# Kernel optimization log

Hardware: AMD Instinct MI355X
Metric: run time of the kernel (lower is better)

Reference implementation:

```python
import jax, jax.numpy as jnp
import numpy as np

B, N, M, D = 64, 512, 1024, 128

def setup_inputs() -> dict:
    key = jax.random.key(0)
    ks = jax.random.split(key, 7)
    s = 1.0 / np.sqrt(D)
    return {
        "h_c": jax.random.normal(ks[0], (B, N, D), dtype=jnp.float32),
        "h_p": jax.random.normal(ks[1], (B, M, D), dtype=jnp.float32),
        "U_w": jax.random.normal(ks[2], (D, D), dtype=jnp.float32) * s,
        "U_b": jax.random.normal(ks[3], (D,), dtype=jnp.float32) * s,
        "V_w": jax.random.normal(ks[4], (D, D), dtype=jnp.float32) * s,
        "V_b": jax.random.normal(ks[5], (D,), dtype=jnp.float32) * s,
        "q": jax.random.normal(ks[6], (D,), dtype=jnp.float32),
    }

def reference(h_c, h_p, U_w, U_b, V_w, V_b, q):
    # ReLU-activated linear projections (torch Linear: x @ W.T + b)
    Uc = jax.nn.relu(jnp.einsum('bnd,ed->bne', h_c, U_w) + U_b)  # (B,N,D)
    Vp = jax.nn.relu(jnp.einsum('bmd,ed->bme', h_p, V_w) + V_b)  # (B,M,D)
    # bilinear attention scores and softmax over protein axis
    attn = jnp.einsum('bnd,bmd->bnm', Uc, Vp)                    # (B,N,M)
    weights = jax.nn.softmax(attn, axis=-1)
    context = jnp.einsum('bnm,bmd->bnd', weights, Vp)            # (B,N,D)
    joint = (Uc + context) * q                                   # (B,N,D)
    return joint.mean(axis=1)                                    # (B,D)
```

## Files before the change

kernel.cpp:

```cpp
#include <hip/hip_runtime.h>
#include <hip/hip_bf16.h>
#include <cstdint>

#define BB 64
#define NN 512
#define MM 1024
#define DD 128

typedef __bf16 bf16x8 __attribute__((ext_vector_type(8)));
typedef float f32x4 __attribute__((ext_vector_type(4)));
typedef short s16x4 __attribute__((ext_vector_type(4)));

static __device__ __forceinline__ unsigned short f2bf(float f) {
    union { float f; unsigned int i; } v; v.f = f;
    unsigned int x = v.i;
    x += 0x7FFFu + ((x >> 16) & 1u);
    return (unsigned short)(x >> 16);
}
static __device__ __forceinline__ unsigned int f2bf2(float a, float b) {
    union { __hip_bfloat162 h; unsigned int u; } c;
    c.h = __float22bfloat162_rn(make_float2(a, b));
    return c.u;
}
static __device__ __forceinline__ void async16(const void* g, void* l) {
    __builtin_amdgcn_global_load_lds(
        (const __attribute__((address_space(1))) void*)g,
        (__attribute__((address_space(3))) void*)l, 16, 0, 0);
}

__global__ __launch_bounds__(256, 4) void proj_kernel(
    const float* __restrict__ hp,
    const float* __restrict__ hc,
    const float* __restrict__ Wu,
    const float* __restrict__ Wv,
    const float* __restrict__ Ub,
    const float* __restrict__ Vb,
    unsigned short* __restrict__ Y,
    unsigned short* __restrict__ YT,
    unsigned short* __restrict__ Ucg,
    float* __restrict__ colsum)
{
    __shared__ __align__(16) unsigned short Ws[128 * 136];
    unsigned short* Ys = Ws;
    unsigned short* Ts = Ws + 8192;
    const int t = threadIdx.x;
    const int lane = t & 63;
    const int wave = t >> 6;
    const int n16 = lane & 15, q = lane >> 4;
    const bool isC = blockIdx.x >= (BB * MM / 64);
    const float ws = isC ? 1.44269504088896f : 1.0f;

    const long row0 = isC ? (long)(blockIdx.x - BB * MM / 64) * 64
                          : (long)blockIdx.x * 64;
    const float* X = isC ? hc : hp;
    const float* Wf = isC ? Wu : Wv;
    const float* bias = isC ? Ub : Vb;

    float4 xv[8];
    {
        const float* xrow = X + (row0 + wave * 16 + n16) * DD + q * 8;
        #pragma unroll
        for (int kk = 0; kk < 4; ++kk) {
            xv[2 * kk]     = *(const float4*)(xrow + kk * 32);
            xv[2 * kk + 1] = *(const float4*)(xrow + kk * 32 + 4);
        }
    }
    {
        const float4* Wg = (const float4*)Wf;
        #pragma unroll
        for (int i = 0; i < 16; ++i) {
            int idx = i * 256 + t;
            float4 v = Wg[idx];
            int off = idx * 4;
            uint2 u = { f2bf2(v.x * ws, v.y * ws), f2bf2(v.z * ws, v.w * ws) };
            *(uint2*)&Ws[(off >> 7) * 136 + (off & 127)] = u;
        }
    }
    __syncthreads();

    f32x4 acc[8];
    #pragma unroll
    for (int j = 0; j < 8; ++j) acc[j] = {0.f, 0.f, 0.f, 0.f};

    #pragma unroll
    for (int kk = 0; kk < 4; ++kk) {
        float4 x0 = xv[2 * kk], x1 = xv[2 * kk + 1];
        union { bf16x8 v; unsigned int u[4]; } a;
        a.u[0] = f2bf2(x0.x, x0.y); a.u[1] = f2bf2(x0.z, x0.w);
        a.u[2] = f2bf2(x1.x, x1.y); a.u[3] = f2bf2(x1.z, x1.w);
        #pragma unroll
        for (int j = 0; j < 8; ++j) {
            bf16x8 b = *(const bf16x8*)&Ws[(j * 16 + n16) * 136 + q * 8 + kk * 32];
            acc[j] = __builtin_amdgcn_mfma_f32_16x16x32_bf16(a.v, b, acc[j], 0, 0, 0);
        }
    }

    unsigned short yb[8][4];
    float colp[8];
    #pragma unroll
    for (int j = 0; j < 8; ++j) {
        const float bv = bias[j * 16 + n16] * ws;
        float y[4], s = 0.f;
        #pragma unroll
        for (int r = 0; r < 4; ++r) {
            float v = acc[j][r] + bv;
            v = v > 0.f ? v : 0.f;
            y[r] = v;
            s += v;
        }
        colp[j] = s;
        uint2 u = { f2bf2(y[0], y[1]), f2bf2(y[2], y[3]) };
        *(uint2*)&yb[j][0] = u;
    }
    __syncthreads();

    if (!isC) {
        #pragma unroll
        for (int j = 0; j < 8; ++j) {
            const int e = j * 16 + n16;
            const int ehi = e >> 3, elo = e & 7;
            #pragma unroll
            for (int r = 0; r < 4; ++r) {
                int row = wave * 16 + q * 4 + r;
                Ys[row * 128 + ((ehi ^ (row & 7)) << 3) + elo] = yb[j][r];
            }
            *(uint2*)&Ts[e * 72 + wave * 16 + q * 4] = *(uint2*)&yb[j][0];
        }
        __syncthreads();
        uint4* dstY = (uint4*)(Y + row0 * DD);
        const long b = row0 >> 10;
        const long mt = (row0 & 1023) >> 6;
        uint4* dstT = (uint4*)(YT + ((b * 16 + mt) * 128) * 64);
        #pragma unroll
        for (int i = 0; i < 4; ++i) {
            int idx = i * 256 + t;
            dstY[idx] = ((const uint4*)Ys)[idx];
            int e = idx >> 3, m = (idx & 7) * 8;
            dstT[idx] = *(const uint4*)&Ts[e * 72 + m];
        }
    } else {
        #pragma unroll
        for (int j = 0; j < 8; ++j) {
            colp[j] += __shfl_xor(colp[j], 16);
            colp[j] += __shfl_xor(colp[j], 32);
        }
        float* cs = (float*)Ts;
        if (q == 0) {
            #pragma unroll
            for (int j = 0; j < 8; ++j)
                cs[wave * 128 + j * 16 + n16] = colp[j];
        }
        #pragma unroll
        for (int j = 0; j < 8; ++j) {
            const int e = j * 16 + n16;
            #pragma unroll
            for (int r = 0; r < 4; ++r)
                Ys[(wave * 16 + q * 4 + r) * 128 + e] = yb[j][r];
        }
        __syncthreads();
        const int c = (int)(row0 >> 6);
        uint4* dstU = (uint4*)(Ucg + row0 * DD);
        #pragma unroll
        for (int i = 0; i < 4; ++i) {
            int idx = i * 256 + t;
            dstU[idx] = ((const uint4*)Ys)[idx];
        }
        if (t < 128)
            colsum[(long)c * DD + t] = cs[t] + cs[128 + t] + cs[256 + t] + cs[384 + t];
    }
}

__global__ __launch_bounds__(256, 2) void attn_kernel(
    const unsigned short* __restrict__ Ucg,
    const unsigned short* __restrict__ Vp,
    const unsigned short* __restrict__ VpT,
    float* __restrict__ part)
{
    __shared__ __align__(16) unsigned short smem[32768];

    const int t = threadIdx.x;
    const int lane = t & 63;
    const int wave = t >> 6;
    const int n16 = lane & 15, q = lane >> 4;

    const int id = blockIdx.x;
    const int xcd = id & 7;
    const int slot = id >> 3;
    const int b = xcd * 8 + (slot >> 3);
    const int nt = slot & 7;

    const unsigned short* vpb = Vp + (long)b * MM * DD;
    const unsigned short* vtb = VpT + (long)b * MM * DD;
    const unsigned short* ucb = Ucg + ((long)b * NN + nt * 64) * DD;

    bf16x8 Bn[4];
    #pragma unroll
    for (int kk = 0; kk < 4; ++kk)
        Bn[kk] = *(const bf16x8*)&ucb[(wave * 16 + n16) * 128 + kk * 32 + q * 8];

    {
        #pragma unroll
        for (int i = 0; i < 4; ++i) {
            int L = wave * 256 + i * 64 + lane;
            async16(vpb + L * 8, smem + wave * 2048 + i * 512);
        }
        #pragma unroll
        for (int i = 0; i < 4; ++i) {
            int L = wave * 256 + i * 64 + lane;
            int r = L >> 3, sc = L & 7, c = sc ^ (r & 7);
            async16(vtb + r * 64 + c * 8, smem + 16384 + wave * 2048 + i * 512);
        }
    }
    asm volatile("s_waitcnt vmcnt(0) lgkmcnt(0)" ::: "memory");
    __builtin_amdgcn_s_barrier();
    __builtin_amdgcn_sched_barrier(0);

    f32x4 O[8];
    #pragma unroll
    for (int j = 0; j < 8; ++j) O[j] = {0.f, 0.f, 0.f, 0.f};
    float lsum = 0.f;

    #pragma unroll 1
    for (int mt = 0; mt < 16; ++mt) {
        const unsigned short* V  = (mt & 1) ? smem + 8192  : smem;
        const unsigned short* VT = (mt & 1) ? smem + 24576 : smem + 16384;
        if (mt < 15) {
            const unsigned short* sv = vpb + (mt + 1) * 8192;
            const unsigned short* st = vtb + (mt + 1) * 8192;
            unsigned short* dv = ((mt & 1) ? smem : smem + 8192) + wave * 2048;
            unsigned short* dt = ((mt & 1) ? smem + 16384 : smem + 24576) + wave * 2048;
            #pragma unroll
            for (int i = 0; i < 4; ++i) {
                int L = wave * 256 + i * 64 + lane;
                async16(sv + L * 8, dv + i * 512);
            }
            #pragma unroll
            for (int i = 0; i < 4; ++i) {
                int L = wave * 256 + i * 64 + lane;
                int r = L >> 3, sc = L & 7, c = sc ^ (r & 7);
                async16(st + r * 64 + c * 8, dt + i * 512);
            }
        }
        __builtin_amdgcn_sched_barrier(0);

        f32x4 S[4];
        #pragma unroll
        for (int j = 0; j < 4; ++j) S[j] = {0.f, 0.f, 0.f, 0.f};
        __builtin_amdgcn_s_setprio(1);
        #pragma unroll
        for (int mtile = 0; mtile < 4; ++mtile) {
            const int m = mtile * 16 + n16;
            #pragma unroll
            for (int kk = 0; kk < 4; ++kk) {
                bf16x8 a = *(const bf16x8*)&V[m * 128 + (((kk * 4 + q) ^ (m & 7)) << 3)];
                S[mtile] = __builtin_amdgcn_mfma_f32_16x16x32_bf16(a, Bn[kk], S[mtile], 0, 0, 0);
            }
        }
        __builtin_amdgcn_s_setprio(0);

        s16x4 av[4];
        #pragma unroll
        for (int j = 0; j < 4; ++j) {
            float p0 = __builtin_exp2f(S[j][0]);
            float p1 = __builtin_exp2f(S[j][1]);
            float p2 = __builtin_exp2f(S[j][2]);
            float p3 = __builtin_exp2f(S[j][3]);
            lsum += (p0 + p1) + (p2 + p3);
            union { unsigned int u[2]; s16x4 v; } pk;
            pk.u[0] = f2bf2(p0, p1); pk.u[1] = f2bf2(p2, p3);
            av[j] = pk.v;
        }

        __builtin_amdgcn_s_setprio(1);
        #pragma unroll
        for (int mtile = 0; mtile < 4; ++mtile) {
            #pragma unroll
            for (int dj = 0; dj < 8; ++dj) {
                const int d = dj * 16 + n16;
                s16x4 bv = *(const s16x4*)&VT[d * 64
                    + (((mtile * 2 + (q >> 1)) ^ (d & 7)) << 3) + ((q & 1) << 2)];
                O[dj] = __builtin_amdgcn_mfma_f32_16x16x16bf16_1k(av[mtile], bv, O[dj], 0, 0, 0);
            }
        }
        __builtin_amdgcn_s_setprio(0);

        asm volatile("s_waitcnt vmcnt(0) lgkmcnt(0)" ::: "memory");
        __builtin_amdgcn_s_barrier();
        __builtin_amdgcn_sched_barrier(0);
    }

    lsum += __shfl_xor(lsum, 16);
    lsum += __shfl_xor(lsum, 32);
    float* scr  = (float*)smem;
    float* invw = scr + wave * 16;
    if (lane < 16) invw[n16] = 1.0f / lsum;
    float iv[4];
    #pragma unroll
    for (int r = 0; r < 4; ++r) iv[r] = invw[q * 4 + r];

    float* red = scr + 64;
    #pragma unroll
    for (int dj = 0; dj < 8; ++dj) {
        float s = O[dj][0] * iv[0] + O[dj][1] * iv[1]
                + O[dj][2] * iv[2] + O[dj][3] * iv[3];
        s += __shfl_xor(s, 16);
        s += __shfl_xor(s, 32);
        if (q == 0)
            red[wave * 128 + dj * 16 + n16] = s;
    }
    __syncthreads();
    if (t < 128) {
        float tot = red[t] + red[128 + t] + red[256 + t] + red[384 + t];
        part[(long)(b * 8 + nt) * DD + t] = tot;
    }
}

__global__ __launch_bounds__(256) void finalize_kernel(
    const float* __restrict__ part, const float* __restrict__ colsum,
    const float* __restrict__ qv, float* __restrict__ out)
{
    int i = blockIdx.x * 256 + threadIdx.x;
    int b = i >> 7, d = i & 127;
    const float* p  = part   + (long)b * 8 * DD + d;
    const float* cs = colsum + (long)b * 8 * DD + d;
    float s = 0.f, u = 0.f;
    #pragma unroll
    for (int nt = 0; nt < 8; ++nt) { s += p[nt * DD]; u += cs[nt * DD]; }
    out[i] = (s + u * 0.69314718055994531f) * qv[d] * (1.0f / (float)NN);
}

extern "C" void kernel_launch(void* const* d_in, const int* in_sizes, int n_in,
                              void* d_out, int out_size, void* d_ws, size_t ws_size,
                              hipStream_t stream) {
    const float* h_c = (const float*)d_in[0];
    const float* h_p = (const float*)d_in[1];
    const float* U_w = (const float*)d_in[2];
    const float* U_b = (const float*)d_in[3];
    const float* V_w = (const float*)d_in[4];
    const float* V_b = (const float*)d_in[5];
    const float* qv  = (const float*)d_in[6];
    float* out = (float*)d_out;

    unsigned short* Vp  = (unsigned short*)d_ws;
    unsigned short* VpT = Vp + (size_t)BB * MM * DD;
    unsigned short* Ucg = VpT + (size_t)BB * MM * DD;
    float* part   = (float*)(Ucg + (size_t)BB * NN * DD);
    float* colsum = part + (size_t)BB * 8 * DD;

    proj_kernel<<<BB * MM / 64 + BB * NN / 64, 256, 0, stream>>>(
        h_p, h_c, U_w, V_w, U_b, V_b, Vp, VpT, Ucg, colsum);
    attn_kernel<<<512, 256, 0, stream>>>(Ucg, Vp, VpT, part);
    finalize_kernel<<<32, 256, 0, stream>>>(part, colsum, qv, out);
}
```

Measured before the change: 136.2 us.

## Make projection kernel persistent with both weights resident and prefetched input tiles

Replaces the 1536-block projection grid with 256 blocks that each process four Vp tiles and two Uc tiles. Both weight matrices are converted to bf16 once per block into swizzled shared memory, and the next tile's inputs are register-prefetched while the current tile computes. This amortises the per-block weight load and conversion and overlaps global loads with MFMA work. In exchange it uses much more LDS (about 98KB), lowers occupancy, and runs with fewer blocks.

Measured after the change: 139.6 us. 2.5% more time.

```diff
diff --git a/kernel.cpp b/kernel.cpp
--- a/kernel.cpp
+++ b/kernel.cpp
@@ -28,7 +28,124 @@
         (__attribute__((address_space(3))) void*)l, 16, 0, 0);
 }
 
-__global__ __launch_bounds__(256, 4) void proj_kernel(
+static __device__ __forceinline__ void loadx(
+    float4 (&xv)[8], const float* __restrict__ base, long row0,
+    int wave, int n16, int q)
+{
+    const float* xrow = base + (row0 + wave * 16 + n16) * DD + q * 8;
+    #pragma unroll
+    for (int kk = 0; kk < 4; ++kk) {
+        xv[2 * kk]     = *(const float4*)(xrow + kk * 32);
+        xv[2 * kk + 1] = *(const float4*)(xrow + kk * 32 + 4);
+    }
+}
+
+template <bool ISC>
+static __device__ __forceinline__ void proj_tile(
+    const float4 (&xv)[8],
+    const unsigned short* Ws,
+    const float* __restrict__ bias,
+    long row0,
+    unsigned short* Ys, unsigned short* Ts,
+    unsigned short* __restrict__ Y, unsigned short* __restrict__ YT,
+    unsigned short* __restrict__ Ucg, float* __restrict__ colsum,
+    int t, int wave, int n16, int q)
+{
+    const float bsc = ISC ? 1.44269504088896f : 1.0f;
+    f32x4 acc[8];
+    #pragma unroll
+    for (int j = 0; j < 8; ++j) acc[j] = {0.f, 0.f, 0.f, 0.f};
+
+    #pragma unroll
+    for (int kk = 0; kk < 4; ++kk) {
+        float4 x0 = xv[2 * kk], x1 = xv[2 * kk + 1];
+        union { bf16x8 v; unsigned int u[4]; } a;
+        a.u[0] = f2bf2(x0.x, x0.y); a.u[1] = f2bf2(x0.z, x0.w);
+        a.u[2] = f2bf2(x1.x, x1.y); a.u[3] = f2bf2(x1.z, x1.w);
+        #pragma unroll
+        for (int j = 0; j < 8; ++j) {
+            bf16x8 b = *(const bf16x8*)&Ws[(j * 16 + n16) * 128
+                                           + (((q + 4 * kk) ^ (n16 & 7)) << 3)];
+            acc[j] = __builtin_amdgcn_mfma_f32_16x16x32_bf16(a.v, b, acc[j], 0, 0, 0);
+        }
+    }
+
+    unsigned short yb[8][4];
+    float colp[8];
+    #pragma unroll
+    for (int j = 0; j < 8; ++j) {
+        const float bv = bias[j * 16 + n16] * bsc;
+        float y[4], s = 0.f;
+        #pragma unroll
+        for (int r = 0; r < 4; ++r) {
+            float v = acc[j][r] + bv;
+            v = v > 0.f ? v : 0.f;
+            y[r] = v;
+            s += v;
+        }
+        colp[j] = s;
+        uint2 u = { f2bf2(y[0], y[1]), f2bf2(y[2], y[3]) };
+        *(uint2*)&yb[j][0] = u;
+    }
+
+    if (!ISC) {
+        #pragma unroll
+        for (int j = 0; j < 8; ++j) {
+            const int e = j * 16 + n16;
+            const int ehi = e >> 3, elo = e & 7;
+            #pragma unroll
+            for (int r = 0; r < 4; ++r) {
+                int row = wave * 16 + q * 4 + r;
+                Ys[row * 128 + ((ehi ^ (row & 7)) << 3) + elo] = yb[j][r];
+            }
+            *(uint2*)&Ts[e * 72 + wave * 16 + q * 4] = *(uint2*)&yb[j][0];
+        }
+        __syncthreads();
+        uint4* dstY = (uint4*)(Y + row0 * DD);
+        uint4* dstT = (uint4*)(YT + row0 * 128);
+        #pragma unroll
+        for (int i = 0; i < 4; ++i) {
+            int idx = i * 256 + t;
+            dstY[idx] = ((const uint4*)Ys)[idx];
+            int e = idx >> 3, m = (idx & 7) * 8;
+            dstT[idx] = *(const uint4*)&Ts[e * 72 + m];
+        }
+        __syncthreads();
+    } else {
+        #pragma unroll
+        for (int j = 0; j < 8; ++j) {
+            colp[j] += __shfl_xor(colp[j], 16);
+            colp[j] += __shfl_xor(colp[j], 32);
+        }
+        float* cs = (float*)Ts;
+        if (q == 0) {
+            #pragma unroll
+            for (int j = 0; j < 8; ++j)
+                cs[wave * 128 + j * 16 + n16] = colp[j];
+        }
+        #pragma unroll
+        for (int j = 0; j < 8; ++j) {
+            const int e = j * 16 + n16;
+            #pragma unroll
+            for (int r = 0; r < 4; ++r)
+                Ys[(wave * 16 + q * 4 + r) * 128 + e] = yb[j][r];
+        }
+        __syncthreads();
+        uint4* dstU = (uint4*)(Ucg + row0 * DD);
+        #pragma unroll
+        for (int i = 0; i < 4; ++i) {
+            int idx = i * 256 + t;
+            dstU[idx] = ((const uint4*)Ys)[idx];
+        }
+        if (t < 128) {
+            int c = (int)(row0 >> 6);
+            colsum[(long)c * DD + t] = cs[t] + cs[128 + t] + cs[256 + t] + cs[384 + t];
+        }
+        __syncthreads();
+    }
+}
+
+__global__ __launch_bounds__(256, 2) void proj_kernel(
     const float* __restrict__ hp,
     const float* __restrict__ hc,
     const float* __restrict__ Wu,
@@ -40,134 +157,60 @@
     unsigned short* __restrict__ Ucg,
     float* __restrict__ colsum)
 {
-    __shared__ __align__(16) unsigned short Ws[128 * 136];
-    unsigned short* Ys = Ws;
-    unsigned short* Ts = Ws + 8192;
+    __shared__ __align__(16) unsigned short S[50176];
+    unsigned short* Wvs = S;
+    unsigned short* Wus = S + 16384;
+    unsigned short* Ys  = S + 32768;
+    unsigned short* Ts  = S + 40960;
+
     const int t = threadIdx.x;
     const int lane = t & 63;
     const int wave = t >> 6;
     const int n16 = lane & 15, q = lane >> 4;
-    const bool isC = blockIdx.x >= (BB * MM / 64);
-    const float ws = isC ? 1.44269504088896f : 1.0f;
-
-    const long row0 = isC ? (long)(blockIdx.x - BB * MM / 64) * 64
-                          : (long)blockIdx.x * 64;
-    const float* X = isC ? hc : hp;
-    const float* Wf = isC ? Wu : Wv;
-    const float* bias = isC ? Ub : Vb;
-
-    float4 xv[8];
+    const int blk = blockIdx.x;
+
+    const long v0 = (long)blk * 4 * 64;
+    const long c0 = (long)blk * 2 * 64;
+
+    float4 xa[8], xb[8];
+    loadx(xa, hp, v0, wave, n16, q);
+
     {
-        const float* xrow = X + (row0 + wave * 16 + n16) * DD + q * 8;
-        #pragma unroll
-        for (int kk = 0; kk < 4; ++kk) {
-            xv[2 * kk]     = *(const float4*)(xrow + kk * 32);
-            xv[2 * kk + 1] = *(const float4*)(xrow + kk * 32 + 4);
-        }
-    }
-    {
-        const float4* Wg = (const float4*)Wf;
+        const float4* Wg = (const float4*)Wv;
         #pragma unroll
         for (int i = 0; i < 16; ++i) {
             int idx = i * 256 + t;
             float4 v = Wg[idx];
-            int off = idx * 4;
-            uint2 u = { f2bf2(v.x * ws, v.y * ws), f2bf2(v.z * ws, v.w * ws) };
-            *(uint2*)&Ws[(off >> 7) * 136 + (off & 127)] = u;
+            int off = idx * 4, r = off >> 7, c = off & 127;
+            uint2 u = { f2bf2(v.x, v.y), f2bf2(v.z, v.w) };
+            *(uint2*)&Wvs[r * 128 + (((c >> 3) ^ (r & 7)) << 3) + (c & 7)] = u;
+        }
+    }
+    {
+        const float4* Wg = (const float4*)Wu;
+        const float s = 1.44269504088896f;
+        #pragma unroll
+        for (int i = 0; i < 16; ++i) {
+            int idx = i * 256 + t;
+            float4 v = Wg[idx];
+            int off = idx * 4, r = off >> 7, c = off & 127;
+            uint2 u = { f2bf2(v.x * s, v.y * s), f2bf2(v.z * s, v.w * s) };
+            *(uint2*)&Wus[r * 128 + (((c >> 3) ^ (r & 7)) << 3) + (c & 7)] = u;
         }
     }
     __syncthreads();
 
-    f32x4 acc[8];
-    #pragma unroll
-    for (int j = 0; j < 8; ++j) acc[j] = {0.f, 0.f, 0.f, 0.f};
-
-    #pragma unroll
-    for (int kk = 0; kk < 4; ++kk) {
-        float4 x0 = xv[2 * kk], x1 = xv[2 * kk + 1];
-        union { bf16x8 v; unsigned int u[4]; } a;
-        a.u[0] = f2bf2(x0.x, x0.y); a.u[1] = f2bf2(x0.z, x0.w);
-        a.u[2] = f2bf2(x1.x, x1.y); a.u[3] = f2bf2(x1.z, x1.w);
-        #pragma unroll
-        for (int j = 0; j < 8; ++j) {
-            bf16x8 b = *(const bf16x8*)&Ws[(j * 16 + n16) * 136 + q * 8 + kk * 32];
-            acc[j] = __builtin_amdgcn_mfma_f32_16x16x32_bf16(a.v, b, acc[j], 0, 0, 0);
-        }
-    }
-
-    unsigned short yb[8][4];
-    float colp[8];
-    #pragma unroll
-    for (int j = 0; j < 8; ++j) {
-        const float bv = bias[j * 16 + n16] * ws;
-        float y[4], s = 0.f;
-        #pragma unroll
-        for (int r = 0; r < 4; ++r) {
-            float v = acc[j][r] + bv;
-            v = v > 0.f ? v : 0.f;
-            y[r] = v;
-            s += v;
-        }
-        colp[j] = s;
-        uint2 u = { f2bf2(y[0], y[1]), f2bf2(y[2], y[3]) };
-        *(uint2*)&yb[j][0] = u;
-    }
-    __syncthreads();
-
-    if (!isC) {
-        #pragma unroll
-        for (int j = 0; j < 8; ++j) {
-            const int e = j * 16 + n16;
-            const int ehi = e >> 3, elo = e & 7;
-            #pragma unroll
-            for (int r = 0; r < 4; ++r) {
-                int row = wave * 16 + q * 4 + r;
-                Ys[row * 128 + ((ehi ^ (row & 7)) << 3) + elo] = yb[j][r];
-            }
-            *(uint2*)&Ts[e * 72 + wave * 16 + q * 4] = *(uint2*)&yb[j][0];
-        }
-        __syncthreads();
-        uint4* dstY = (uint4*)(Y + row0 * DD);
-        const long b = row0 >> 10;
-        const long mt = (row0 & 1023) >> 6;
-        uint4* dstT = (uint4*)(YT + ((b * 16 + mt) * 128) * 64);
-        #pragma unroll
-        for (int i = 0; i < 4; ++i) {
-            int idx = i * 256 + t;
-            dstY[idx] = ((const uint4*)Ys)[idx];
-            int e = idx >> 3, m = (idx & 7) * 8;
-            dstT[idx] = *(const uint4*)&Ts[e * 72 + m];
-        }
-    } else {
-        #pragma unroll
-        for (int j = 0; j < 8; ++j) {
-            colp[j] += __shfl_xor(colp[j], 16);
-            colp[j] += __shfl_xor(colp[j], 32);
-        }
-        float* cs = (float*)Ts;
-        if (q == 0) {
-            #pragma unroll
-            for (int j = 0; j < 8; ++j)
-                cs[wave * 128 + j * 16 + n16] = colp[j];
-        }
-        #pragma unroll
-        for (int j = 0; j < 8; ++j) {
-            const int e = j * 16 + n16;
-            #pragma unroll
-            for (int r = 0; r < 4; ++r)
-                Ys[(wave * 16 + q * 4 + r) * 128 + e] = yb[j][r];
-        }
-        __syncthreads();
-        const int c = (int)(row0 >> 6);
-        uint4* dstU = (uint4*)(Ucg + row0 * DD);
-        #pragma unroll
-        for (int i = 0; i < 4; ++i) {
-            int idx = i * 256 + t;
-            dstU[idx] = ((const uint4*)Ys)[idx];
-        }
-        if (t < 128)
-            colsum[(long)c * DD + t] = cs[t] + cs[128 + t] + cs[256 + t] + cs[384 + t];
-    }
+    loadx(xb, hp, v0 + 64, wave, n16, q);
+    proj_tile<false>(xa, Wvs, Vb, v0,       Ys, Ts, Y, YT, Ucg, colsum, t, wave, n16, q);
+    loadx(xa, hp, v0 + 128, wave, n16, q);
+    proj_tile<false>(xb, Wvs, Vb, v0 + 64,  Ys, Ts, Y, YT, Ucg, colsum, t, wave, n16, q);
+    loadx(xb, hp, v0 + 192, wave, n16, q);
+    proj_tile<false>(xa, Wvs, Vb, v0 + 128, Ys, Ts, Y, YT, Ucg, colsum, t, wave, n16, q);
+    loadx(xa, hc, c0, wave, n16, q);
+    proj_tile<false>(xb, Wvs, Vb, v0 + 192, Ys, Ts, Y, YT, Ucg, colsum, t, wave, n16, q);
+    loadx(xb, hc, c0 + 64, wave, n16, q);
+    proj_tile<true>(xa, Wus, Ub, c0,        Ys, Ts, Y, YT, Ucg, colsum, t, wave, n16, q);
+    proj_tile<true>(xb, Wus, Ub, c0 + 64,   Ys, Ts, Y, YT, Ucg, colsum, t, wave, n16, q);
 }
 
 __global__ __launch_bounds__(256, 2) void attn_kernel(
@@ -347,7 +390,7 @@
     float* part   = (float*)(Ucg + (size_t)BB * NN * DD);
     float* colsum = part + (size_t)BB * 8 * DD;
 
-    proj_kernel<<<BB * MM / 64 + BB * NN / 64, 256, 0, stream>>>(
+    proj_kernel<<<256, 256, 0, stream>>>(
         h_p, h_c, U_w, V_w, U_b, V_b, Vp, VpT, Ucg, colsum);
     attn_kernel<<<512, 256, 0, stream>>>(Ucg, Vp, VpT, part);
     finalize_kernel<<<32, 256, 0, stream>>>(part, colsum, qv, out);
```
